# Kernel optimization log

Measured on AMD Instinct MI355X. Metric: run time of the kernel, lower is better.

The kernel has to match this reference:

```python
import jax, jax.numpy as jnp
import numpy as np

N, E, D_IN, D_H, N_CLASSES = 50000, 800000, 128, 128, 40
D_OUT = D_H // 2
LN_EPS = 1e-5


def _seg_mean(msgs, dst, n_nodes):
    # mean aggregation over incoming edges; isolated nodes get 0 (like PyG mean)
    s = jax.ops.segment_sum(msgs, dst, num_segments=n_nodes)
    cnt = jax.ops.segment_sum(jnp.ones((dst.shape[0], 1), msgs.dtype), dst, num_segments=n_nodes)
    return s / jnp.maximum(cnt, 1.0)


def _sage(x, src, dst, Wl, bl, Wr):
    # PyG SAGEConv(mean): lin_l(mean_j x_j) + lin_r(x_i); lin_l has bias, lin_r none
    agg = _seg_mean(x[src], dst, x.shape[0])  # [N, d_in]
    return agg @ Wl + bl + x @ Wr


def _layernorm(x, g, b):
    mu = jnp.mean(x, axis=-1, keepdims=True)
    var = jnp.mean(jnp.square(x - mu), axis=-1, keepdims=True)
    return (x - mu) * jax.lax.rsqrt(var + LN_EPS) * g + b


def setup_inputs() -> dict:
    key = jax.random.key(0)
    ks = jax.random.split(key, 20)
    sc = lambda d: 1.0 / np.sqrt(d)
    inp = {
        "x": jax.random.normal(ks[0], (N, D_IN), dtype=jnp.float32),
        "edge_index": jax.random.randint(ks[1], (2, E), 0, N, dtype=jnp.int32),
        # block1 (in==hidden -> proj is Identity)
        "Wl1": jax.random.normal(ks[2], (D_IN, D_H), jnp.float32) * sc(D_IN),
        "bl1": jnp.zeros((D_H,), jnp.float32),
        "Wr1": jax.random.normal(ks[3], (D_IN, D_H), jnp.float32) * sc(D_IN),
        "g1": jnp.ones((D_H,), jnp.float32),
        "b1": jnp.zeros((D_H,), jnp.float32),
        # block2
        "Wl2": jax.random.normal(ks[4], (D_H, D_H), jnp.float32) * sc(D_H),
        "bl2": jnp.zeros((D_H,), jnp.float32),
        "Wr2": jax.random.normal(ks[5], (D_H, D_H), jnp.float32) * sc(D_H),
        "g2": jnp.ones((D_H,), jnp.float32),
        "b2": jnp.zeros((D_H,), jnp.float32),
        # conv_out: hidden -> hidden//2
        "Wl3": jax.random.normal(ks[6], (D_H, D_OUT), jnp.float32) * sc(D_H),
        "bl3": jnp.zeros((D_OUT,), jnp.float32),
        "Wr3": jax.random.normal(ks[7], (D_H, D_OUT), jnp.float32) * sc(D_H),
        # classifier: LayerNorm(D_OUT) + Linear(D_OUT, n_classes)
        "gc": jnp.ones((D_OUT,), jnp.float32),
        "bc": jnp.zeros((D_OUT,), jnp.float32),
        "Wc": jax.random.normal(ks[8], (D_OUT, N_CLASSES), jnp.float32) * sc(D_OUT),
        "bcls": jnp.zeros((N_CLASSES,), jnp.float32),
    }
    return inp


def reference(x, edge_index, Wl1, bl1, Wr1, g1, b1, Wl2, bl2, Wr2, g2, b2,
              Wl3, bl3, Wr3, gc, bc, Wc, bcls):
    src, dst = edge_index[0], edge_index[1]
    # block1: SAGE -> LN -> GELU -> (dropout eval=identity) -> +x (proj=Identity)
    h = _sage(x, src, dst, Wl1, bl1, Wr1)
    x = jax.nn.gelu(_layernorm(h, g1, b1), approximate=False) + x
    # block2
    h = _sage(x, src, dst, Wl2, bl2, Wr2)
    x = jax.nn.gelu(_layernorm(h, g2, b2), approximate=False) + x
    # conv_out + GELU
    x = jax.nn.gelu(_sage(x, src, dst, Wl3, bl3, Wr3), approximate=False)
    # classifier: LN then Linear
    return _layernorm(x, gc, bc) @ Wc + bcls
```

## Files before the change

kernel.cpp:

```cpp
#include <hip/hip_runtime.h>
#include <math.h>


typedef __attribute__((ext_vector_type(8))) short bf16x8;
typedef __attribute__((ext_vector_type(4))) float f32x4;

#define NWG 256
#define NBK 196
#define CAP2 6144

__device__ inline float gelu_f(float x) {
    float u = x * (1.0f + 0.044715f * x * x);
    return x / (1.0f + __expf(-1.5957691216057308f * u));
}

__device__ inline ushort f2b(float f) {
    uint u = __float_as_uint(f);
    u += 0x7fffu + ((u >> 16) & 1u);
    return (ushort)(u >> 16);
}

__device__ inline float b2f(ushort h) { return __uint_as_float((uint)h << 16); }


__global__ __launch_bounds__(256) void k_hist(const int* __restrict__ dst, int e,
                                              int* __restrict__ cnts) {
    __shared__ int h[NBK];
    const int tid = threadIdx.x;
    const int wg = blockIdx.x;
    for (int i = tid; i < NBK; i += 256) h[i] = 0;
    __syncthreads();
    const int ch = (e + NWG - 1) / NWG;
    const int lo = wg * ch;
    const int hi = min(e, lo + ch);
    for (int i = lo + tid; i < hi; i += 256) atomicAdd(&h[dst[i] >> 8], 1);
    __syncthreads();
    for (int i = tid; i < NBK; i += 256) cnts[i * NWG + wg] = h[i];
}

__global__ __launch_bounds__(256) void k_scanP1(const int* __restrict__ in,
                                                int* __restrict__ out,
                                                int* __restrict__ part, int m) {
    __shared__ int sm[256];
    const int tid = threadIdx.x;
    const int base = blockIdx.x * 1024 + tid * 4;
    int4 v = make_int4(0, 0, 0, 0);
    if (base + 3 < m) {
        v = *(const int4*)(in + base);
    } else {
        if (base + 0 < m) v.x = in[base + 0];
        if (base + 1 < m) v.y = in[base + 1];
        if (base + 2 < m) v.z = in[base + 2];
        if (base + 3 < m) v.w = in[base + 3];
    }
    int s = v.x + v.y + v.z + v.w;
    sm[tid] = s;
    __syncthreads();
#pragma unroll
    for (int d = 1; d < 256; d <<= 1) {
        int add = (tid >= d) ? sm[tid - d] : 0;
        __syncthreads();
        sm[tid] += add;
        __syncthreads();
    }
    int ex = (tid ? sm[tid - 1] : 0);
    if (base + 0 < m) out[base + 0] = ex;
    ex += v.x;
    if (base + 1 < m) out[base + 1] = ex;
    ex += v.y;
    if (base + 2 < m) out[base + 2] = ex;
    ex += v.z;
    if (base + 3 < m) out[base + 3] = ex;
    if (tid == 255) part[blockIdx.x] = sm[255];
}

__global__ __launch_bounds__(256) void k_scanP2(int* __restrict__ out,
                                                const int* __restrict__ part, int m) {
    const int tid = threadIdx.x;
    const int bid = blockIdx.x;
    const int lane = tid & 63;
    int s = 0;
    for (int j = lane; j < bid; j += 64) s += part[j];
#pragma unroll
    for (int d = 32; d > 0; d >>= 1) s += __shfl_xor(s, d);
    const int i0 = bid * 1024 + tid * 4;
#pragma unroll
    for (int j = 0; j < 4; ++j) {
        int i = i0 + j;
        if (i < m) out[i] += s;
    }
}

__global__ __launch_bounds__(256) void k_scat(const int* __restrict__ src,
                                              const int* __restrict__ dst, int e,
                                              const int* __restrict__ bases,
                                              uint* __restrict__ pairs) {
    __shared__ int cur[NBK];
    const int tid = threadIdx.x;
    const int wg = blockIdx.x;
    for (int i = tid; i < NBK; i += 256) cur[i] = bases[i * NWG + wg];
    __syncthreads();
    const int ch = (e + NWG - 1) / NWG;
    const int lo = wg * ch;
    const int hi = min(e, lo + ch);
    for (int i = lo + tid; i < hi; i += 256) {
        int d = dst[i];
        int pos = atomicAdd(&cur[d >> 8], 1);
        pairs[pos] = (uint)src[i] | ((uint)(d & 255) << 16);
    }
}

__global__ __launch_bounds__(256) void k_sortC(const uint* __restrict__ pairs,
                                               const int* __restrict__ bases, int e,
                                               int* __restrict__ csr, int* __restrict__ off,
                                               int* __restrict__ cntout, int n) {
    __shared__ int hist[256];
    __shared__ int curl[256];
    __shared__ int sm[256];
    __shared__ int buf[CAP2];
    const int bk = blockIdx.x;
    const int tid = threadIdx.x;
    const int start = bases[bk * NWG];
    const int end = (bk == NBK - 1) ? e : bases[(bk + 1) * NWG];
    int m = end - start;
    if (m > CAP2) m = CAP2;

    hist[tid] = 0;
    __syncthreads();
    for (int i = tid; i < m; i += 256) atomicAdd(&hist[(pairs[start + i] >> 16) & 255], 1);
    __syncthreads();
    int v = hist[tid];
    sm[tid] = v;
    __syncthreads();
#pragma unroll
    for (int d = 1; d < 256; d <<= 1) {
        int add = (tid >= d) ? sm[tid - d] : 0;
        __syncthreads();
        sm[tid] += add;
        __syncthreads();
    }
    int excl = sm[tid] - v;
    int node = (bk << 8) + tid;
    if (node < n) {
        off[node] = start + excl;
        cntout[node] = v;
    }
    curl[tid] = excl;
    __syncthreads();
    for (int i = tid; i < m; i += 256) {
        uint w = pairs[start + i];
        int pos = atomicAdd(&curl[(w >> 16) & 255], 1);
        buf[pos] = (int)(w & 0xffffu);
    }
    __syncthreads();
    for (int i = tid; i < m; i += 256) csr[start + i] = buf[i];
}


__global__ void k_cast(const float* __restrict__ in, ushort* __restrict__ out, int nvec4) {
    int t = blockIdx.x * blockDim.x + threadIdx.x;
    int stride = gridDim.x * blockDim.x;
    for (int i = t; i < nvec4; i += stride) {
        float4 v = ((const float4*)in)[i];
        ushort4 o;
        o.x = f2b(v.x);
        o.y = f2b(v.y);
        o.z = f2b(v.z);
        o.w = f2b(v.w);
        ((ushort4*)out)[i] = o;
    }
}

__global__ void k_wprep(const float* __restrict__ Wl, const float* __restrict__ Wr,
                        int KH, int C, ushort* __restrict__ Wt) {
    int t = blockIdx.x * blockDim.x + threadIdx.x;
    int total = C * 2 * KH;
    if (t >= total) return;
    int c = t / (2 * KH), k = t % (2 * KH);
    float v = (k < KH) ? Wl[(size_t)k * C + c] : Wr[(size_t)(k - KH) * C + c];
    Wt[t] = f2b(v);
}

__global__ void k_wprepC(const float* __restrict__ Wc, ushort* __restrict__ Wct) {
    int t = blockIdx.x * blockDim.x + threadIdx.x;
    if (t >= 64 * 64) return;
    int c = t >> 6, k = t & 63;
    float v = (c < 40) ? Wc[k * 40 + c] : 0.f;
    Wct[t] = f2b(v);
}


__global__ __launch_bounds__(256) void k_agg(const ushort* __restrict__ X,
                                             const int* __restrict__ off,
                                             const int* __restrict__ cnt,
                                             const int* __restrict__ csr,
                                             ushort* __restrict__ agg, int n) {
    const int wave = threadIdx.x >> 6;
    const int lane = threadIdx.x & 63;
    const int base = blockIdx.x * 32 + wave * 8;
#pragma unroll 1
    for (int j = 0; j < 8; ++j) {
        const int i = base + j;
        if (i >= n) return;
        int s0 = off[i];
        int deg = cnt[i];
        int c = 0;
        if (lane < deg) c = csr[s0 + lane];
        float a0 = 0.f, a1 = 0.f;
        const int dcap = deg < 64 ? deg : 64;
        int t = 0;
        for (; t + 3 < dcap; t += 4) {
            int i0 = __shfl(c, t), i1 = __shfl(c, t + 1);
            int i2 = __shfl(c, t + 2), i3 = __shfl(c, t + 3);
            uint u0 = *((const uint*)(X + (size_t)i0 * 128) + lane);
            uint u1 = *((const uint*)(X + (size_t)i1 * 128) + lane);
            uint u2 = *((const uint*)(X + (size_t)i2 * 128) + lane);
            uint u3 = *((const uint*)(X + (size_t)i3 * 128) + lane);
            a0 += __uint_as_float(u0 << 16) + __uint_as_float(u1 << 16) +
                  __uint_as_float(u2 << 16) + __uint_as_float(u3 << 16);
            a1 += __uint_as_float(u0 & 0xffff0000u) + __uint_as_float(u1 & 0xffff0000u) +
                  __uint_as_float(u2 & 0xffff0000u) + __uint_as_float(u3 & 0xffff0000u);
        }
        for (; t < dcap; ++t) {
            uint u0 = *((const uint*)(X + (size_t)__shfl(c, t) * 128) + lane);
            a0 += __uint_as_float(u0 << 16);
            a1 += __uint_as_float(u0 & 0xffff0000u);
        }
        for (int tt = s0 + 64; tt < s0 + deg; ++tt) {
            uint u0 = *((const uint*)(X + (size_t)csr[tt] * 128) + lane);
            a0 += __uint_as_float(u0 << 16);
            a1 += __uint_as_float(u0 & 0xffff0000u);
        }
        float inv = 1.0f / (float)(deg > 1 ? deg : 1);
        uint pk = (uint)f2b(a0 * inv) | ((uint)f2b(a1 * inv) << 16);
        *((uint*)(agg + (size_t)i * 128) + lane) = pk;
    }
}


template <int DOUT, int EPI>
__global__ __launch_bounds__(256) void k_gemm(
    const ushort* __restrict__ Agg, const ushort* __restrict__ Xb,
    const ushort* __restrict__ Wt, const float* __restrict__ bias,
    const float* __restrict__ g, const float* __restrict__ b,
    ushort* __restrict__ OutB, int n) {
    constexpr int CT = DOUT / 64;
    const int tid = threadIdx.x;
    const int wave = tid >> 6;
    const int lane = tid & 63;
    const int l16 = lane & 15;
    const int g4 = lane >> 4;
    const int row0 = blockIdx.x * 32;

    __shared__ __align__(16) ushort As[32 * 256];

    int colv[CT];
#pragma unroll
    for (int ct = 0; ct < CT; ++ct) colv[ct] = (wave * CT + ct) * 16 + l16;

    bf16x8 bfr[CT][8];
#pragma unroll
    for (int ct = 0; ct < CT; ++ct) {
        const ushort* wp = Wt + (size_t)colv[ct] * 256 + g4 * 8;
#pragma unroll
        for (int ks = 0; ks < 8; ++ks) bfr[ct][ks] = *(const bf16x8*)(wp + ks * 32);
    }

    {
        const int row = tid >> 3;
        const int jj = tid & 7;
        int gr = row0 + row;
        if (gr > n - 1) gr = n - 1;
        const ushort* pa = Agg + (size_t)gr * 128;
        const ushort* pb = Xb + (size_t)gr * 128;
        uint4 v0 = *(const uint4*)(pa + jj * 8);
        uint4 v1 = *(const uint4*)(pa + (jj + 8) * 8);
        uint4 v2 = *(const uint4*)(pb + jj * 8);
        uint4 v3 = *(const uint4*)(pb + (jj + 8) * 8);
        const int sw = (row & 7) << 4;
        char* lb = (char*)As + row * 512;
        *(uint4*)(lb + ((jj * 16) ^ sw)) = v0;
        *(uint4*)(lb + (((jj + 8) * 16) ^ sw)) = v1;
        *(uint4*)(lb + (((jj + 16) * 16) ^ sw)) = v2;
        *(uint4*)(lb + (((jj + 24) * 16) ^ sw)) = v3;
    }

    float biasv[CT], gv[CT], bbv[CT];
#pragma unroll
    for (int ct = 0; ct < CT; ++ct) {
        biasv[ct] = bias[colv[ct]];
        gv[ct] = g[colv[ct]];
        bbv[ct] = b[colv[ct]];
    }

    __syncthreads();

    f32x4 acc[2][CT];
#pragma unroll
    for (int rt = 0; rt < 2; ++rt)
#pragma unroll
        for (int ct = 0; ct < CT; ++ct) {
            acc[rt][ct][0] = 0.f;
            acc[rt][ct][1] = 0.f;
            acc[rt][ct][2] = 0.f;
            acc[rt][ct][3] = 0.f;
        }
#pragma unroll
    for (int ks = 0; ks < 8; ++ks) {
        bf16x8 a[2];
#pragma unroll
        for (int rt = 0; rt < 2; ++rt) {
            const int row = rt * 16 + l16;
            a[rt] = *(const bf16x8*)((const char*)As + row * 512 +
                                     ((ks * 64 + g4 * 16) ^ ((row & 7) << 4)));
        }
#pragma unroll
        for (int rt = 0; rt < 2; ++rt)
#pragma unroll
            for (int ct = 0; ct < CT; ++ct)
                acc[rt][ct] = __builtin_amdgcn_mfma_f32_16x16x32_bf16(a[rt], bfr[ct][ks],
                                                                     acc[rt][ct], 0, 0, 0);
    }

    __shared__ float sP[32][4];
    __shared__ float qP[32][4];
    float v[2][4][CT];
    float sv[2][4], qv[2][4];
#pragma unroll
    for (int rt = 0; rt < 2; ++rt)
#pragma unroll
        for (int reg = 0; reg < 4; ++reg) {
            float s = 0.f, q = 0.f;
#pragma unroll
            for (int ct = 0; ct < CT; ++ct) {
                float t = acc[rt][ct][reg] + biasv[ct];
                if (EPI == 3) t = gelu_f(t);
                v[rt][reg][ct] = t;
                s += t;
                q += t * t;
            }
            sv[rt][reg] = s;
            qv[rt][reg] = q;
        }
#pragma unroll
    for (int m = 1; m < 16; m <<= 1)
#pragma unroll
        for (int rt = 0; rt < 2; ++rt)
#pragma unroll
            for (int reg = 0; reg < 4; ++reg) {
                sv[rt][reg] += __shfl_xor(sv[rt][reg], m);
                qv[rt][reg] += __shfl_xor(qv[rt][reg], m);
            }
    if (l16 == 0) {
#pragma unroll
        for (int rt = 0; rt < 2; ++rt)
#pragma unroll
            for (int reg = 0; reg < 4; ++reg) {
                int rib = rt * 16 + g4 * 4 + reg;
                sP[rib][wave] = sv[rt][reg];
                qP[rib][wave] = qv[rt][reg];
            }
    }
    __syncthreads();
#pragma unroll
    for (int rt = 0; rt < 2; ++rt) {
#pragma unroll
        for (int reg = 0; reg < 4; ++reg) {
            int rib = rt * 16 + g4 * 4 + reg;
            float s = sP[rib][0] + sP[rib][1] + sP[rib][2] + sP[rib][3];
            float q = qP[rib][0] + qP[rib][1] + qP[rib][2] + qP[rib][3];
            float mu = s * (1.0f / (float)DOUT);
            float var = q * (1.0f / (float)DOUT) - mu * mu;
            float rs = rsqrtf(fmaxf(var, 0.f) + 1e-5f);
            int r = row0 + rib;
            if (r >= n) continue;
#pragma unroll
            for (int ct = 0; ct < CT; ++ct) {
                float y = (v[rt][reg][ct] - mu) * rs * gv[ct] + bbv[ct];
                if (EPI == 1) {
                    ushort rh = *(const ushort*)((const char*)As + rib * 512 +
                                                 ((256 + 2 * colv[ct]) ^ ((rib & 7) << 4)));
                    y = gelu_f(y) + b2f(rh);
                }
                OutB[(size_t)r * DOUT + colv[ct]] = f2b(y);
            }
        }
    }
}


__global__ __launch_bounds__(256) void k_mm(const ushort* __restrict__ Y,
                                            const ushort* __restrict__ Wct,
                                            const float* __restrict__ bcls,
                                            float* __restrict__ Out, int n) {
    const int tid = threadIdx.x;
    const int wave = tid >> 6;
    const int lane = tid & 63;
    const int l16 = lane & 15;
    const int g4 = lane >> 4;
    const int row0 = blockIdx.x * 32;
    const int col = wave * 16 + l16;

    bf16x8 bfr[2];
#pragma unroll
    for (int ks = 0; ks < 2; ++ks)
        bfr[ks] = *(const bf16x8*)(Wct + (size_t)col * 64 + ks * 32 + g4 * 8);

    f32x4 acc[2];
#pragma unroll
    for (int rt = 0; rt < 2; ++rt) {
        acc[rt][0] = 0.f;
        acc[rt][1] = 0.f;
        acc[rt][2] = 0.f;
        acc[rt][3] = 0.f;
    }

    int arow[2];
#pragma unroll
    for (int rt = 0; rt < 2; ++rt) {
        int r = row0 + rt * 16 + l16;
        arow[rt] = (r < n) ? r : (n - 1);
    }

#pragma unroll
    for (int ks = 0; ks < 2; ++ks)
#pragma unroll
        for (int rt = 0; rt < 2; ++rt) {
            bf16x8 a = *(const bf16x8*)(Y + (size_t)arow[rt] * 64 + ks * 32 + g4 * 8);
            acc[rt] = __builtin_amdgcn_mfma_f32_16x16x32_bf16(a, bfr[ks], acc[rt], 0, 0, 0);
        }

    const float bcv = (col < 40) ? bcls[col] : 0.f;
#pragma unroll
    for (int rt = 0; rt < 2; ++rt)
#pragma unroll
        for (int reg = 0; reg < 4; ++reg) {
            int r = row0 + rt * 16 + g4 * 4 + reg;
            if (r < n && col < 40) Out[(size_t)r * 40 + col] = acc[rt][reg] + bcv;
        }
}


extern "C" void kernel_launch(void* const* d_in, const int* in_sizes, int n_in,
                              void* d_out, int out_size, void* d_ws, size_t ws_size,
                              hipStream_t stream) {
    const float* x   = (const float*)d_in[0];
    const int* ei    = (const int*)d_in[1];
    const float* Wl1 = (const float*)d_in[2];
    const float* bl1 = (const float*)d_in[3];
    const float* Wr1 = (const float*)d_in[4];
    const float* g1  = (const float*)d_in[5];
    const float* b1  = (const float*)d_in[6];
    const float* Wl2 = (const float*)d_in[7];
    const float* bl2 = (const float*)d_in[8];
    const float* Wr2 = (const float*)d_in[9];
    const float* g2  = (const float*)d_in[10];
    const float* b2  = (const float*)d_in[11];
    const float* Wl3 = (const float*)d_in[12];
    const float* bl3 = (const float*)d_in[13];
    const float* Wr3 = (const float*)d_in[14];
    const float* gc  = (const float*)d_in[15];
    const float* bc  = (const float*)d_in[16];
    const float* Wc  = (const float*)d_in[17];
    const float* bcls= (const float*)d_in[18];

    const int n = in_sizes[0] / 128;
    const int e = in_sizes[1] / 2;
    const int* src = ei;
    const int* dst = ei + e;

    char* w = (char*)d_ws;
    size_t o = 0;
    auto alloc = [&](size_t bytes) -> char* {
        char* p = w + o;
        o = (o + bytes + 511) & ~(size_t)511;
        return p;
    };
    int* cnts    = (int*)alloc((size_t)NBK * NWG * 4);
    int* bases   = (int*)alloc((size_t)NBK * NWG * 4);
    int* part    = (int*)alloc(256 * 4);
    uint* pairs  = (uint*)alloc((size_t)e * 4);
    int* csr     = (int*)alloc((size_t)e * 4);
    int* off     = (int*)alloc((size_t)n * 4);
    int* cnt     = (int*)alloc((size_t)n * 4);
    ushort* xB   = (ushort*)alloc((size_t)n * 128 * 2);
    ushort* aggB = (ushort*)alloc((size_t)n * 128 * 2);
    ushort* xaB  = (ushort*)alloc((size_t)n * 128 * 2);
    ushort* xbB  = (ushort*)alloc((size_t)n * 128 * 2);
    ushort* yB   = (ushort*)alloc((size_t)n * 64 * 2);
    ushort* W1t  = (ushort*)alloc((size_t)128 * 256 * 2);
    ushort* W2t  = (ushort*)alloc((size_t)128 * 256 * 2);
    ushort* W3t  = (ushort*)alloc((size_t)64 * 256 * 2);
    ushort* Wct  = (ushort*)alloc((size_t)64 * 64 * 2);
    (void)ws_size;

    const int m = NBK * NWG;
    const int sblk = (m + 1023) / 1024;
    k_hist<<<NWG, 256, 0, stream>>>(dst, e, cnts);
    k_scanP1<<<sblk, 256, 0, stream>>>(cnts, bases, part, m);
    k_scanP2<<<sblk, 256, 0, stream>>>(bases, part, m);
    k_scat<<<NWG, 256, 0, stream>>>(src, dst, e, bases, pairs);
    k_sortC<<<NBK, 256, 0, stream>>>(pairs, bases, e, csr, off, cnt, n);

    k_cast<<<2048, 256, 0, stream>>>(x, xB, n * 128 / 4);
    k_wprep<<<(128 * 256 + 255) / 256, 256, 0, stream>>>(Wl1, Wr1, 128, 128, W1t);
    k_wprep<<<(128 * 256 + 255) / 256, 256, 0, stream>>>(Wl2, Wr2, 128, 128, W2t);
    k_wprep<<<(64 * 256 + 255) / 256, 256, 0, stream>>>(Wl3, Wr3, 128, 64, W3t);
    k_wprepC<<<16, 256, 0, stream>>>(Wc, Wct);

    const int gg = (n + 31) / 32;

    k_agg<<<gg, 256, 0, stream>>>(xB, off, cnt, csr, aggB, n);
    k_gemm<128, 1><<<gg, 256, 0, stream>>>(aggB, xB, W1t, bl1, g1, b1, xaB, n);
    k_agg<<<gg, 256, 0, stream>>>(xaB, off, cnt, csr, aggB, n);
    k_gemm<128, 1><<<gg, 256, 0, stream>>>(aggB, xaB, W2t, bl2, g2, b2, xbB, n);
    k_agg<<<gg, 256, 0, stream>>>(xbB, off, cnt, csr, aggB, n);
    k_gemm<64, 3><<<gg, 256, 0, stream>>>(aggB, xbB, W3t, bl3, gc, bc, yB, n);
    k_mm<<<gg, 256, 0, stream>>>(yB, Wct, bcls, (float*)d_out, n);
}
```

Before: 207.5 us.

## Process two row tiles per GEMM block with prefetched double-buffered LDS

Each k_gemm block now handles 64 rows as two 32-row tiles instead of one. The weight fragments held in registers are loaded once and reused for both tiles. The second tile's global loads are issued into registers while the first tile is being computed, and each tile gets its own LDS buffer. This targets the per-block cost of reloading weights and overlaps global memory latency with MFMA and epilogue work, at the price of a halved grid, more LDS, and higher register pressure.

Result: slower. 223.7 us (+7.8%).

```diff
diff --git a/kernel.cpp b/kernel.cpp
--- a/kernel.cpp
+++ b/kernel.cpp
@@ -250,9 +250,10 @@
     const int lane = tid & 63;
     const int l16 = lane & 15;
     const int g4 = lane >> 4;
-    const int row0 = blockIdx.x * 32;
-
-    __shared__ __align__(16) ushort As[32 * 256];
+
+    __shared__ __align__(16) ushort As[2][32 * 256];
+    __shared__ float sP[32][4];
+    __shared__ float qP[32][4];
 
     int colv[CT];
 #pragma unroll
@@ -265,26 +266,6 @@
 #pragma unroll
         for (int ks = 0; ks < 8; ++ks) bfr[ct][ks] = *(const bf16x8*)(wp + ks * 32);
     }
-
-    {
-        const int row = tid >> 3;
-        const int jj = tid & 7;
-        int gr = row0 + row;
-        if (gr > n - 1) gr = n - 1;
-        const ushort* pa = Agg + (size_t)gr * 128;
-        const ushort* pb = Xb + (size_t)gr * 128;
-        uint4 v0 = *(const uint4*)(pa + jj * 8);
-        uint4 v1 = *(const uint4*)(pa + (jj + 8) * 8);
-        uint4 v2 = *(const uint4*)(pb + jj * 8);
-        uint4 v3 = *(const uint4*)(pb + (jj + 8) * 8);
-        const int sw = (row & 7) << 4;
-        char* lb = (char*)As + row * 512;
-        *(uint4*)(lb + ((jj * 16) ^ sw)) = v0;
-        *(uint4*)(lb + (((jj + 8) * 16) ^ sw)) = v1;
-        *(uint4*)(lb + (((jj + 16) * 16) ^ sw)) = v2;
-        *(uint4*)(lb + (((jj + 24) * 16) ^ sw)) = v3;
-    }
-
     float biasv[CT], gv[CT], bbv[CT];
 #pragma unroll
     for (int ct = 0; ct < CT; ++ct) {
@@ -293,96 +274,123 @@
         bbv[ct] = b[colv[ct]];
     }
 
-    __syncthreads();
-
-    f32x4 acc[2][CT];
-#pragma unroll
-    for (int rt = 0; rt < 2; ++rt)
-#pragma unroll
-        for (int ct = 0; ct < CT; ++ct) {
-            acc[rt][ct][0] = 0.f;
-            acc[rt][ct][1] = 0.f;
-            acc[rt][ct][2] = 0.f;
-            acc[rt][ct][3] = 0.f;
-        }
-#pragma unroll
-    for (int ks = 0; ks < 8; ++ks) {
-        bf16x8 a[2];
+    const int srow = tid >> 3;
+    const int sjj = tid & 7;
+    auto ldtile = [&](int row0, uint4* v) {
+        int gr = row0 + srow;
+        if (gr > n - 1) gr = n - 1;
+        const ushort* pa = Agg + (size_t)gr * 128;
+        const ushort* pb = Xb + (size_t)gr * 128;
+        v[0] = *(const uint4*)(pa + sjj * 8);
+        v[1] = *(const uint4*)(pa + (sjj + 8) * 8);
+        v[2] = *(const uint4*)(pb + sjj * 8);
+        v[3] = *(const uint4*)(pb + (sjj + 8) * 8);
+    };
+
+    uint4 ld[4];
+    ldtile(blockIdx.x * 64, ld);
+
+#pragma unroll
+    for (int t = 0; t < 2; ++t) {
+        const int row0 = blockIdx.x * 64 + t * 32;
+        {
+            const int sw = (srow & 7) << 4;
+            char* lb = (char*)As[t] + srow * 512;
+            *(uint4*)(lb + ((sjj * 16) ^ sw)) = ld[0];
+            *(uint4*)(lb + (((sjj + 8) * 16) ^ sw)) = ld[1];
+            *(uint4*)(lb + (((sjj + 16) * 16) ^ sw)) = ld[2];
+            *(uint4*)(lb + (((sjj + 24) * 16) ^ sw)) = ld[3];
+        }
+        if (t == 0) ldtile(blockIdx.x * 64 + 32, ld);
+        __syncthreads();
+
+        f32x4 acc[2][CT];
+#pragma unroll
+        for (int rt = 0; rt < 2; ++rt)
+#pragma unroll
+            for (int ct = 0; ct < CT; ++ct) {
+                acc[rt][ct][0] = 0.f;
+                acc[rt][ct][1] = 0.f;
+                acc[rt][ct][2] = 0.f;
+                acc[rt][ct][3] = 0.f;
+            }
+#pragma unroll
+        for (int ks = 0; ks < 8; ++ks) {
+            bf16x8 a[2];
+#pragma unroll
+            for (int rt = 0; rt < 2; ++rt) {
+                const int row = rt * 16 + l16;
+                a[rt] = *(const bf16x8*)((const char*)As[t] + row * 512 +
+                                         ((ks * 64 + g4 * 16) ^ ((row & 7) << 4)));
+            }
+#pragma unroll
+            for (int rt = 0; rt < 2; ++rt)
+#pragma unroll
+                for (int ct = 0; ct < CT; ++ct)
+                    acc[rt][ct] = __builtin_amdgcn_mfma_f32_16x16x32_bf16(a[rt], bfr[ct][ks],
+                                                                         acc[rt][ct], 0, 0, 0);
+        }
+
+        float v[2][4][CT];
+        float sv[2][4], qv[2][4];
+#pragma unroll
+        for (int rt = 0; rt < 2; ++rt)
+#pragma unroll
+            for (int reg = 0; reg < 4; ++reg) {
+                float s = 0.f, q = 0.f;
+#pragma unroll
+                for (int ct = 0; ct < CT; ++ct) {
+                    float tv = acc[rt][ct][reg] + biasv[ct];
+                    if (EPI == 3) tv = gelu_f(tv);
+                    v[rt][reg][ct] = tv;
+                    s += tv;
+                    q += tv * tv;
+                }
+                sv[rt][reg] = s;
+                qv[rt][reg] = q;
+            }
+#pragma unroll
+        for (int m = 1; m < 16; m <<= 1)
+#pragma unroll
+            for (int rt = 0; rt < 2; ++rt)
+#pragma unroll
+                for (int reg = 0; reg < 4; ++reg) {
+                    sv[rt][reg] += __shfl_xor(sv[rt][reg], m);
+                    qv[rt][reg] += __shfl_xor(qv[rt][reg], m);
+                }
+        if (l16 == 0) {
+#pragma unroll
+            for (int rt = 0; rt < 2; ++rt)
+#pragma unroll
+                for (int reg = 0; reg < 4; ++reg) {
+                    int rib = rt * 16 + g4 * 4 + reg;
+                    sP[rib][wave] = sv[rt][reg];
+                    qP[rib][wave] = qv[rt][reg];
+                }
+        }
+        __syncthreads();
 #pragma unroll
         for (int rt = 0; rt < 2; ++rt) {
-            const int row = rt * 16 + l16;
-            a[rt] = *(const bf16x8*)((const char*)As + row * 512 +
-                                     ((ks * 64 + g4 * 16) ^ ((row & 7) << 4)));
-        }
-#pragma unroll
-        for (int rt = 0; rt < 2; ++rt)
-#pragma unroll
-            for (int ct = 0; ct < CT; ++ct)
-                acc[rt][ct] = __builtin_amdgcn_mfma_f32_16x16x32_bf16(a[rt], bfr[ct][ks],
-                                                                     acc[rt][ct], 0, 0, 0);
-    }
-
-    __shared__ float sP[32][4];
-    __shared__ float qP[32][4];
-    float v[2][4][CT];
-    float sv[2][4], qv[2][4];
-#pragma unroll
-    for (int rt = 0; rt < 2; ++rt)
-#pragma unroll
-        for (int reg = 0; reg < 4; ++reg) {
-            float s = 0.f, q = 0.f;
-#pragma unroll
-            for (int ct = 0; ct < CT; ++ct) {
-                float t = acc[rt][ct][reg] + biasv[ct];
-                if (EPI == 3) t = gelu_f(t);
-                v[rt][reg][ct] = t;
-                s += t;
-                q += t * t;
-            }
-            sv[rt][reg] = s;
-            qv[rt][reg] = q;
-        }
-#pragma unroll
-    for (int m = 1; m < 16; m <<= 1)
-#pragma unroll
-        for (int rt = 0; rt < 2; ++rt)
-#pragma unroll
-            for (int reg = 0; reg < 4; ++reg) {
-                sv[rt][reg] += __shfl_xor(sv[rt][reg], m);
-                qv[rt][reg] += __shfl_xor(qv[rt][reg], m);
-            }
-    if (l16 == 0) {
-#pragma unroll
-        for (int rt = 0; rt < 2; ++rt)
 #pragma unroll
             for (int reg = 0; reg < 4; ++reg) {
                 int rib = rt * 16 + g4 * 4 + reg;
-                sP[rib][wave] = sv[rt][reg];
-                qP[rib][wave] = qv[rt][reg];
-            }
-    }
-    __syncthreads();
-#pragma unroll
-    for (int rt = 0; rt < 2; ++rt) {
-#pragma unroll
-        for (int reg = 0; reg < 4; ++reg) {
-            int rib = rt * 16 + g4 * 4 + reg;
-            float s = sP[rib][0] + sP[rib][1] + sP[rib][2] + sP[rib][3];
-            float q = qP[rib][0] + qP[rib][1] + qP[rib][2] + qP[rib][3];
-            float mu = s * (1.0f / (float)DOUT);
-            float var = q * (1.0f / (float)DOUT) - mu * mu;
-            float rs = rsqrtf(fmaxf(var, 0.f) + 1e-5f);
-            int r = row0 + rib;
-            if (r >= n) continue;
-#pragma unroll
-            for (int ct = 0; ct < CT; ++ct) {
-                float y = (v[rt][reg][ct] - mu) * rs * gv[ct] + bbv[ct];
-                if (EPI == 1) {
-                    ushort rh = *(const ushort*)((const char*)As + rib * 512 +
-                                                 ((256 + 2 * colv[ct]) ^ ((rib & 7) << 4)));
-                    y = gelu_f(y) + b2f(rh);
+                float s = sP[rib][0] + sP[rib][1] + sP[rib][2] + sP[rib][3];
+                float q = qP[rib][0] + qP[rib][1] + qP[rib][2] + qP[rib][3];
+                float mu = s * (1.0f / (float)DOUT);
+                float var = q * (1.0f / (float)DOUT) - mu * mu;
+                float rs = rsqrtf(fmaxf(var, 0.f) + 1e-5f);
+                int r = row0 + rib;
+                if (r >= n) continue;
+#pragma unroll
+                for (int ct = 0; ct < CT; ++ct) {
+                    float y = (v[rt][reg][ct] - mu) * rs * gv[ct] + bbv[ct];
+                    if (EPI == 1) {
+                        ushort rh = *(const ushort*)((const char*)As[t] + rib * 512 +
+                                                     ((256 + 2 * colv[ct]) ^ ((rib & 7) << 4)));
+                        y = gelu_f(y) + b2f(rh);
+                    }
+                    OutB[(size_t)r * DOUT + colv[ct]] = f2b(y);
                 }
-                OutB[(size_t)r * DOUT + colv[ct]] = f2b(y);
             }
         }
     }
@@ -508,13 +516,14 @@
     k_wprep<<<(64 * 256 + 255) / 256, 256, 0, stream>>>(Wl3, Wr3, 128, 64, W3t);
     k_wprepC<<<16, 256, 0, stream>>>(Wc, Wct);
 
-    const int gg = (n + 31) / 32;
-
-    k_agg<<<gg, 256, 0, stream>>>(xB, off, cnt, csr, aggB, n);
+    const int ga = (n + 31) / 32;
+    const int gg = (n + 63) / 64;
+
+    k_agg<<<ga, 256, 0, stream>>>(xB, off, cnt, csr, aggB, n);
     k_gemm<128, 1><<<gg, 256, 0, stream>>>(aggB, xB, W1t, bl1, g1, b1, xaB, n);
-    k_agg<<<gg, 256, 0, stream>>>(xaB, off, cnt, csr, aggB, n);
+    k_agg<<<ga, 256, 0, stream>>>(xaB, off, cnt, csr, aggB, n);
     k_gemm<128, 1><<<gg, 256, 0, stream>>>(aggB, xaB, W2t, bl2, g2, b2, xbB, n);
-    k_agg<<<gg, 256, 0, stream>>>(xbB, off, cnt, csr, aggB, n);
+    k_agg<<<ga, 256, 0, stream>>>(xbB, off, cnt, csr, aggB, n);
     k_gemm<64, 3><<<gg, 256, 0, stream>>>(aggB, xbB, W3t, bl3, gc, bc, yB, n);
-    k_mm<<<gg, 256, 0, stream>>>(yB, Wct, bcls, (float*)d_out, n);
-}
+    k_mm<<<ga, 256, 0, stream>>>(yB, Wct, bcls, (float*)d_out, n);
+}
```

## Fuse classifier matmul into final SAGE gemm and use direct global-to-LDS loads

Applied to the files above, without the earlier changes.

Fuses the final classifier Linear into the third gemm kernel's epilogue. The LayerNorm output is staged in a swizzled LDS tile and multiplied there, which removes the intermediate yB buffer and one kernel launch. Also replaces the register-staged A-tile load with global_load_lds direct-to-LDS transfers, swizzling on the source address. This adds LDS use and a barrier in the EPI==3 kernel, and relies on correct vmcnt waiting before the LDS reads.

New measurement: 202.0 us. 1.03x faster.

```diff
diff --git a/kernel.cpp b/kernel.cpp
--- a/kernel.cpp
+++ b/kernel.cpp
@@ -4,6 +4,9 @@
 
 typedef __attribute__((ext_vector_type(8))) short bf16x8;
 typedef __attribute__((ext_vector_type(4))) float f32x4;
+
+#define AS1 __attribute__((address_space(1)))
+#define AS3 __attribute__((address_space(3)))
 
 #define NWG 256
 #define NBK 196
@@ -243,7 +246,11 @@
     const ushort* __restrict__ Agg, const ushort* __restrict__ Xb,
     const ushort* __restrict__ Wt, const float* __restrict__ bias,
     const float* __restrict__ g, const float* __restrict__ b,
-    ushort* __restrict__ OutB, int n) {
+    ushort* __restrict__ OutB,
+    const ushort* __restrict__ Wct,
+    const float* __restrict__ bcls,
+    float* __restrict__ OutF,
+    int n) {
     constexpr int CT = DOUT / 64;
     const int tid = threadIdx.x;
     const int wave = tid >> 6;
@@ -253,6 +260,25 @@
     const int row0 = blockIdx.x * 32;
 
     __shared__ __align__(16) ushort As[32 * 256];
+    __shared__ float sP[32][4];
+    __shared__ float qP[32][4];
+    __shared__ __align__(16) ushort Ys[EPI == 3 ? 32 * 64 : 1];
+
+    {
+        const int slot = lane & 31;
+#pragma unroll
+        for (int i = 0; i < 4; ++i) {
+            const int rr = (wave * 4 + i) * 2 + (lane >> 5);
+            int gr = row0 + rr;
+            if (gr > n - 1) gr = n - 1;
+            const int srcb = (slot * 16) ^ ((rr & 7) << 4);
+            const char* gp = (srcb < 256)
+                                 ? (const char*)Agg + (size_t)gr * 256 + srcb
+                                 : (const char*)Xb + (size_t)gr * 256 + (srcb - 256);
+            char* lp = (char*)As + (wave * 4 + i) * 1024;
+            __builtin_amdgcn_global_load_lds((const AS1 void*)gp, (AS3 void*)lp, 16, 0, 0);
+        }
+    }
 
     int colv[CT];
 #pragma unroll
@@ -265,26 +291,6 @@
 #pragma unroll
         for (int ks = 0; ks < 8; ++ks) bfr[ct][ks] = *(const bf16x8*)(wp + ks * 32);
     }
-
-    {
-        const int row = tid >> 3;
-        const int jj = tid & 7;
-        int gr = row0 + row;
-        if (gr > n - 1) gr = n - 1;
-        const ushort* pa = Agg + (size_t)gr * 128;
-        const ushort* pb = Xb + (size_t)gr * 128;
-        uint4 v0 = *(const uint4*)(pa + jj * 8);
-        uint4 v1 = *(const uint4*)(pa + (jj + 8) * 8);
-        uint4 v2 = *(const uint4*)(pb + jj * 8);
-        uint4 v3 = *(const uint4*)(pb + (jj + 8) * 8);
-        const int sw = (row & 7) << 4;
-        char* lb = (char*)As + row * 512;
-        *(uint4*)(lb + ((jj * 16) ^ sw)) = v0;
-        *(uint4*)(lb + (((jj + 8) * 16) ^ sw)) = v1;
-        *(uint4*)(lb + (((jj + 16) * 16) ^ sw)) = v2;
-        *(uint4*)(lb + (((jj + 24) * 16) ^ sw)) = v3;
-    }
-
     float biasv[CT], gv[CT], bbv[CT];
 #pragma unroll
     for (int ct = 0; ct < CT; ++ct) {
@@ -322,8 +328,6 @@
                                                                      acc[rt][ct], 0, 0, 0);
     }
 
-    __shared__ float sP[32][4];
-    __shared__ float qP[32][4];
     float v[2][4][CT];
     float sv[2][4], qv[2][4];
 #pragma unroll
@@ -333,11 +337,11 @@
             float s = 0.f, q = 0.f;
 #pragma unroll
             for (int ct = 0; ct < CT; ++ct) {
-                float t = acc[rt][ct][reg] + biasv[ct];
-                if (EPI == 3) t = gelu_f(t);
-                v[rt][reg][ct] = t;
-                s += t;
-                q += t * t;
+                float tv = acc[rt][ct][reg] + biasv[ct];
+                if (EPI == 3) tv = gelu_f(tv);
+                v[rt][reg][ct] = tv;
+                s += tv;
+                q += tv * tv;
             }
             sv[rt][reg] = s;
             qv[rt][reg] = q;
@@ -362,6 +366,7 @@
             }
     }
     __syncthreads();
+
 #pragma unroll
     for (int rt = 0; rt < 2; ++rt) {
 #pragma unroll
@@ -373,71 +378,57 @@
             float var = q * (1.0f / (float)DOUT) - mu * mu;
             float rs = rsqrtf(fmaxf(var, 0.f) + 1e-5f);
             int r = row0 + rib;
-            if (r >= n) continue;
 #pragma unroll
             for (int ct = 0; ct < CT; ++ct) {
                 float y = (v[rt][reg][ct] - mu) * rs * gv[ct] + bbv[ct];
                 if (EPI == 1) {
-                    ushort rh = *(const ushort*)((const char*)As + rib * 512 +
-                                                 ((256 + 2 * colv[ct]) ^ ((rib & 7) << 4)));
-                    y = gelu_f(y) + b2f(rh);
+                    if (r < n) {
+                        ushort rh = *(const ushort*)((const char*)As + rib * 512 +
+                                                     ((256 + 2 * colv[ct]) ^ ((rib & 7) << 4)));
+                        y = gelu_f(y) + b2f(rh);
+                        OutB[(size_t)r * DOUT + colv[ct]] = f2b(y);
+                    }
+                } else {
+                    *(ushort*)((char*)Ys + rib * 128 +
+                               ((2 * colv[ct]) ^ ((rib & 7) << 4))) = f2b(y);
                 }
-                OutB[(size_t)r * DOUT + colv[ct]] = f2b(y);
             }
         }
     }
-}
-
-
-__global__ __launch_bounds__(256) void k_mm(const ushort* __restrict__ Y,
-                                            const ushort* __restrict__ Wct,
-                                            const float* __restrict__ bcls,
-                                            float* __restrict__ Out, int n) {
-    const int tid = threadIdx.x;
-    const int wave = tid >> 6;
-    const int lane = tid & 63;
-    const int l16 = lane & 15;
-    const int g4 = lane >> 4;
-    const int row0 = blockIdx.x * 32;
-    const int col = wave * 16 + l16;
-
-    bf16x8 bfr[2];
-#pragma unroll
-    for (int ks = 0; ks < 2; ++ks)
-        bfr[ks] = *(const bf16x8*)(Wct + (size_t)col * 64 + ks * 32 + g4 * 8);
-
-    f32x4 acc[2];
-#pragma unroll
-    for (int rt = 0; rt < 2; ++rt) {
-        acc[rt][0] = 0.f;
-        acc[rt][1] = 0.f;
-        acc[rt][2] = 0.f;
-        acc[rt][3] = 0.f;
-    }
-
-    int arow[2];
-#pragma unroll
-    for (int rt = 0; rt < 2; ++rt) {
-        int r = row0 + rt * 16 + l16;
-        arow[rt] = (r < n) ? r : (n - 1);
-    }
-
-#pragma unroll
-    for (int ks = 0; ks < 2; ++ks)
+
+    if (EPI == 3) {
+        __syncthreads();
+        const int col = wave * 16 + l16;
+        bf16x8 b2r[2];
+#pragma unroll
+        for (int ks = 0; ks < 2; ++ks)
+            b2r[ks] = *(const bf16x8*)(Wct + (size_t)col * 64 + ks * 32 + g4 * 8);
+        f32x4 acc2[2];
 #pragma unroll
         for (int rt = 0; rt < 2; ++rt) {
-            bf16x8 a = *(const bf16x8*)(Y + (size_t)arow[rt] * 64 + ks * 32 + g4 * 8);
-            acc[rt] = __builtin_amdgcn_mfma_f32_16x16x32_bf16(a, bfr[ks], acc[rt], 0, 0, 0);
-        }
-
-    const float bcv = (col < 40) ? bcls[col] : 0.f;
-#pragma unroll
-    for (int rt = 0; rt < 2; ++rt)
-#pragma unroll
-        for (int reg = 0; reg < 4; ++reg) {
-            int r = row0 + rt * 16 + g4 * 4 + reg;
-            if (r < n && col < 40) Out[(size_t)r * 40 + col] = acc[rt][reg] + bcv;
-        }
+            acc2[rt][0] = 0.f;
+            acc2[rt][1] = 0.f;
+            acc2[rt][2] = 0.f;
+            acc2[rt][3] = 0.f;
+        }
+#pragma unroll
+        for (int ks = 0; ks < 2; ++ks)
+#pragma unroll
+            for (int rt = 0; rt < 2; ++rt) {
+                const int row = rt * 16 + l16;
+                bf16x8 a = *(const bf16x8*)((const char*)Ys + row * 128 +
+                                            ((ks * 64 + g4 * 16) ^ ((row & 7) << 4)));
+                acc2[rt] = __builtin_amdgcn_mfma_f32_16x16x32_bf16(a, b2r[ks], acc2[rt], 0, 0, 0);
+            }
+        const float bcv = (col < 40) ? bcls[col] : 0.f;
+#pragma unroll
+        for (int rt = 0; rt < 2; ++rt)
+#pragma unroll
+            for (int reg = 0; reg < 4; ++reg) {
+                int r = row0 + rt * 16 + g4 * 4 + reg;
+                if (r < n && col < 40) OutF[(size_t)r * 40 + col] = acc2[rt][reg] + bcv;
+            }
+    }
 }
 
 
@@ -487,7 +478,6 @@
     ushort* aggB = (ushort*)alloc((size_t)n * 128 * 2);
     ushort* xaB  = (ushort*)alloc((size_t)n * 128 * 2);
     ushort* xbB  = (ushort*)alloc((size_t)n * 128 * 2);
-    ushort* yB   = (ushort*)alloc((size_t)n * 64 * 2);
     ushort* W1t  = (ushort*)alloc((size_t)128 * 256 * 2);
     ushort* W2t  = (ushort*)alloc((size_t)128 * 256 * 2);
     ushort* W3t  = (ushort*)alloc((size_t)64 * 256 * 2);
@@ -511,10 +501,12 @@
     const int gg = (n + 31) / 32;
 
     k_agg<<<gg, 256, 0, stream>>>(xB, off, cnt, csr, aggB, n);
-    k_gemm<128, 1><<<gg, 256, 0, stream>>>(aggB, xB, W1t, bl1, g1, b1, xaB, n);
+    k_gemm<128, 1><<<gg, 256, 0, stream>>>(aggB, xB, W1t, bl1, g1, b1, xaB,
+                                           nullptr, nullptr, nullptr, n);
     k_agg<<<gg, 256, 0, stream>>>(xaB, off, cnt, csr, aggB, n);
-    k_gemm<128, 1><<<gg, 256, 0, stream>>>(aggB, xaB, W2t, bl2, g2, b2, xbB, n);
+    k_gemm<128, 1><<<gg, 256, 0, stream>>>(aggB, xaB, W2t, bl2, g2, b2, xbB,
+                                           nullptr, nullptr, nullptr, n);
     k_agg<<<gg, 256, 0, stream>>>(xbB, off, cnt, csr, aggB, n);
-    k_gemm<64, 3><<<gg, 256, 0, stream>>>(aggB, xbB, W3t, bl3, gc, bc, yB, n);
-    k_mm<<<gg, 256, 0, stream>>>(yB, Wct, bcls, (float*)d_out, n);
-}
+    k_gemm<64, 3><<<gg, 256, 0, stream>>>(aggB, xbB, W3t, bl3, gc, bc, nullptr,
+                                          Wct, bcls, (float*)d_out, n);
+}
```

## Reorder SAGE layers to transform first, then aggregate with fused LayerNorm epilogue

Applied to the files above, without the earlier changes.

Uses the linearity of mean aggregation to compute X@[Wl|Wr] first, in a plain MFMA GEMM that writes a wide bf16 intermediate. Neighbour aggregation then runs on the projected features, and bias, LayerNorm, GELU and the residual are fused into that gather kernel using wave-level reductions. In the third layer the gather reads 64-wide rows instead of 128-wide ones, which cuts the dominant irregular memory traffic. The cost is writing a wider intermediate, strided gathers over 512-byte rows, and rounding to bf16 before aggregation, which slightly changes numerics.

Result: slower. 220.2 us (+6.1%).

```diff
diff --git a/kernel.cpp b/kernel.cpp
--- a/kernel.cpp
+++ b/kernel.cpp
@@ -4,6 +4,9 @@
 
 typedef __attribute__((ext_vector_type(8))) short bf16x8;
 typedef __attribute__((ext_vector_type(4))) float f32x4;
+
+#define AS1 __attribute__((address_space(1)))
+#define AS3 __attribute__((address_space(3)))
 
 #define NWG 256
 #define NBK 196
@@ -12,6 +15,12 @@
 __device__ inline float gelu_f(float x) {
     float u = x * (1.0f + 0.044715f * x * x);
     return x / (1.0f + __expf(-1.5957691216057308f * u));
+}
+
+__device__ inline float wave_sum(float v) {
+#pragma unroll
+    for (int d = 32; d > 0; d >>= 1) v += __shfl_xor(v, d);
+    return v;
 }
 
 __device__ inline ushort f2b(float f) {
@@ -171,13 +180,13 @@
     }
 }
 
-__global__ void k_wprep(const float* __restrict__ Wl, const float* __restrict__ Wr,
-                        int KH, int C, ushort* __restrict__ Wt) {
+__global__ void k_wprepW(const float* __restrict__ Wl, const float* __restrict__ Wr,
+                         int CH, int K, ushort* __restrict__ Wt) {
     int t = blockIdx.x * blockDim.x + threadIdx.x;
-    int total = C * 2 * KH;
+    int total = 2 * CH * K;
     if (t >= total) return;
-    int c = t / (2 * KH), k = t % (2 * KH);
-    float v = (k < KH) ? Wl[(size_t)k * C + c] : Wr[(size_t)(k - KH) * C + c];
+    int c = t / K, k = t % K;
+    float v = (c < CH) ? Wl[(size_t)k * CH + c] : Wr[(size_t)k * CH + (c - CH)];
     Wt[t] = f2b(v);
 }
 
@@ -190,14 +199,103 @@
 }
 
 
-__global__ __launch_bounds__(256) void k_agg(const ushort* __restrict__ X,
-                                             const int* __restrict__ off,
-                                             const int* __restrict__ cnt,
-                                             const int* __restrict__ csr,
-                                             ushort* __restrict__ agg, int n) {
+template <int CW>
+__global__ __launch_bounds__(256) void k_gemmW(const ushort* __restrict__ X,
+                                               const ushort* __restrict__ Wt,
+                                               ushort* __restrict__ Y, int n) {
+    constexpr int CT = CW / 64;
+    const int tid = threadIdx.x;
+    const int wave = tid >> 6;
+    const int lane = tid & 63;
+    const int l16 = lane & 15;
+    const int g4 = lane >> 4;
+    const int row0 = blockIdx.x * 32;
+
+    __shared__ __align__(16) ushort As[32 * 128];
+
+    {
+        const int slot = lane & 15;
+#pragma unroll
+        for (int i = 0; i < 2; ++i) {
+            const int rr = (wave * 2 + i) * 4 + (lane >> 4);
+            int gr = row0 + rr;
+            if (gr > n - 1) gr = n - 1;
+            const int srcb = (slot * 16) ^ ((rr & 7) << 4);
+            const char* gp = (const char*)X + (size_t)gr * 256 + srcb;
+            char* lp = (char*)As + (wave * 2 + i) * 1024;
+            __builtin_amdgcn_global_load_lds((const AS1 void*)gp, (AS3 void*)lp, 16, 0, 0);
+        }
+    }
+
+    int colv[CT];
+#pragma unroll
+    for (int ct = 0; ct < CT; ++ct) colv[ct] = (wave * CT + ct) * 16 + l16;
+
+    bf16x8 bfr[CT][4];
+#pragma unroll
+    for (int ct = 0; ct < CT; ++ct) {
+        const ushort* wp = Wt + (size_t)colv[ct] * 128 + g4 * 8;
+#pragma unroll
+        for (int ks = 0; ks < 4; ++ks) bfr[ct][ks] = *(const bf16x8*)(wp + ks * 32);
+    }
+
+    __syncthreads();
+
+    f32x4 acc[2][CT];
+#pragma unroll
+    for (int rt = 0; rt < 2; ++rt)
+#pragma unroll
+        for (int ct = 0; ct < CT; ++ct) {
+            acc[rt][ct][0] = 0.f;
+            acc[rt][ct][1] = 0.f;
+            acc[rt][ct][2] = 0.f;
+            acc[rt][ct][3] = 0.f;
+        }
+#pragma unroll
+    for (int ks = 0; ks < 4; ++ks) {
+        bf16x8 a[2];
+#pragma unroll
+        for (int rt = 0; rt < 2; ++rt) {
+            const int row = rt * 16 + l16;
+            a[rt] = *(const bf16x8*)((const char*)As + row * 256 +
+                                     ((ks * 64 + g4 * 16) ^ ((row & 7) << 4)));
+        }
+#pragma unroll
+        for (int rt = 0; rt < 2; ++rt)
+#pragma unroll
+            for (int ct = 0; ct < CT; ++ct)
+                acc[rt][ct] = __builtin_amdgcn_mfma_f32_16x16x32_bf16(a[rt], bfr[ct][ks],
+                                                                     acc[rt][ct], 0, 0, 0);
+    }
+
+#pragma unroll
+    for (int rt = 0; rt < 2; ++rt)
+#pragma unroll
+        for (int reg = 0; reg < 4; ++reg) {
+            int r = row0 + rt * 16 + g4 * 4 + reg;
+            if (r >= n) continue;
+#pragma unroll
+            for (int ct = 0; ct < CT; ++ct)
+                Y[(size_t)r * CW + colv[ct]] = f2b(acc[rt][ct][reg]);
+        }
+}
+
+
+__global__ __launch_bounds__(256) void k_aggpost(
+    const ushort* __restrict__ Y,
+    const ushort* __restrict__ Xres,
+    const int* __restrict__ off, const int* __restrict__ cnt,
+    const int* __restrict__ csr, const float* __restrict__ bl,
+    const float* __restrict__ g, const float* __restrict__ b,
+    ushort* __restrict__ Xout, int n) {
     const int wave = threadIdx.x >> 6;
     const int lane = threadIdx.x & 63;
     const int base = blockIdx.x * 32 + wave * 8;
+
+    const float2 blv = ((const float2*)bl)[lane];
+    const float2 gv = ((const float2*)g)[lane];
+    const float2 bv = ((const float2*)b)[lane];
+
 #pragma unroll 1
     for (int j = 0; j < 8; ++j) {
         const int i = base + j;
@@ -212,179 +310,84 @@
         for (; t + 3 < dcap; t += 4) {
             int i0 = __shfl(c, t), i1 = __shfl(c, t + 1);
             int i2 = __shfl(c, t + 2), i3 = __shfl(c, t + 3);
-            uint u0 = *((const uint*)(X + (size_t)i0 * 128) + lane);
-            uint u1 = *((const uint*)(X + (size_t)i1 * 128) + lane);
-            uint u2 = *((const uint*)(X + (size_t)i2 * 128) + lane);
-            uint u3 = *((const uint*)(X + (size_t)i3 * 128) + lane);
+            uint u0 = *((const uint*)(Y + (size_t)i0 * 256) + lane);
+            uint u1 = *((const uint*)(Y + (size_t)i1 * 256) + lane);
+            uint u2 = *((const uint*)(Y + (size_t)i2 * 256) + lane);
+            uint u3 = *((const uint*)(Y + (size_t)i3 * 256) + lane);
             a0 += __uint_as_float(u0 << 16) + __uint_as_float(u1 << 16) +
                   __uint_as_float(u2 << 16) + __uint_as_float(u3 << 16);
             a1 += __uint_as_float(u0 & 0xffff0000u) + __uint_as_float(u1 & 0xffff0000u) +
                   __uint_as_float(u2 & 0xffff0000u) + __uint_as_float(u3 & 0xffff0000u);
         }
         for (; t < dcap; ++t) {
-            uint u0 = *((const uint*)(X + (size_t)__shfl(c, t) * 128) + lane);
+            uint u0 = *((const uint*)(Y + (size_t)__shfl(c, t) * 256) + lane);
             a0 += __uint_as_float(u0 << 16);
             a1 += __uint_as_float(u0 & 0xffff0000u);
         }
         for (int tt = s0 + 64; tt < s0 + deg; ++tt) {
-            uint u0 = *((const uint*)(X + (size_t)csr[tt] * 128) + lane);
+            uint u0 = *((const uint*)(Y + (size_t)csr[tt] * 256) + lane);
             a0 += __uint_as_float(u0 << 16);
             a1 += __uint_as_float(u0 & 0xffff0000u);
         }
         float inv = 1.0f / (float)(deg > 1 ? deg : 1);
-        uint pk = (uint)f2b(a0 * inv) | ((uint)f2b(a1 * inv) << 16);
-        *((uint*)(agg + (size_t)i * 128) + lane) = pk;
-    }
-}
-
-
-template <int DOUT, int EPI>
-__global__ __launch_bounds__(256) void k_gemm(
-    const ushort* __restrict__ Agg, const ushort* __restrict__ Xb,
-    const ushort* __restrict__ Wt, const float* __restrict__ bias,
-    const float* __restrict__ g, const float* __restrict__ b,
-    ushort* __restrict__ OutB, int n) {
-    constexpr int CT = DOUT / 64;
-    const int tid = threadIdx.x;
-    const int wave = tid >> 6;
-    const int lane = tid & 63;
-    const int l16 = lane & 15;
-    const int g4 = lane >> 4;
-    const int row0 = blockIdx.x * 32;
-
-    __shared__ __align__(16) ushort As[32 * 256];
-
-    int colv[CT];
-#pragma unroll
-    for (int ct = 0; ct < CT; ++ct) colv[ct] = (wave * CT + ct) * 16 + l16;
-
-    bf16x8 bfr[CT][8];
-#pragma unroll
-    for (int ct = 0; ct < CT; ++ct) {
-        const ushort* wp = Wt + (size_t)colv[ct] * 256 + g4 * 8;
-#pragma unroll
-        for (int ks = 0; ks < 8; ++ks) bfr[ct][ks] = *(const bf16x8*)(wp + ks * 32);
-    }
-
-    {
-        const int row = tid >> 3;
-        const int jj = tid & 7;
-        int gr = row0 + row;
-        if (gr > n - 1) gr = n - 1;
-        const ushort* pa = Agg + (size_t)gr * 128;
-        const ushort* pb = Xb + (size_t)gr * 128;
-        uint4 v0 = *(const uint4*)(pa + jj * 8);
-        uint4 v1 = *(const uint4*)(pa + (jj + 8) * 8);
-        uint4 v2 = *(const uint4*)(pb + jj * 8);
-        uint4 v3 = *(const uint4*)(pb + (jj + 8) * 8);
-        const int sw = (row & 7) << 4;
-        char* lb = (char*)As + row * 512;
-        *(uint4*)(lb + ((jj * 16) ^ sw)) = v0;
-        *(uint4*)(lb + (((jj + 8) * 16) ^ sw)) = v1;
-        *(uint4*)(lb + (((jj + 16) * 16) ^ sw)) = v2;
-        *(uint4*)(lb + (((jj + 24) * 16) ^ sw)) = v3;
-    }
-
-    float biasv[CT], gv[CT], bbv[CT];
-#pragma unroll
-    for (int ct = 0; ct < CT; ++ct) {
-        biasv[ct] = bias[colv[ct]];
-        gv[ct] = g[colv[ct]];
-        bbv[ct] = b[colv[ct]];
-    }
-
-    __syncthreads();
-
-    f32x4 acc[2][CT];
-#pragma unroll
-    for (int rt = 0; rt < 2; ++rt)
-#pragma unroll
-        for (int ct = 0; ct < CT; ++ct) {
-            acc[rt][ct][0] = 0.f;
-            acc[rt][ct][1] = 0.f;
-            acc[rt][ct][2] = 0.f;
-            acc[rt][ct][3] = 0.f;
-        }
-#pragma unroll
-    for (int ks = 0; ks < 8; ++ks) {
-        bf16x8 a[2];
-#pragma unroll
-        for (int rt = 0; rt < 2; ++rt) {
-            const int row = rt * 16 + l16;
-            a[rt] = *(const bf16x8*)((const char*)As + row * 512 +
-                                     ((ks * 64 + g4 * 16) ^ ((row & 7) << 4)));
-        }
-#pragma unroll
-        for (int rt = 0; rt < 2; ++rt)
-#pragma unroll
-            for (int ct = 0; ct < CT; ++ct)
-                acc[rt][ct] = __builtin_amdgcn_mfma_f32_16x16x32_bf16(a[rt], bfr[ct][ks],
-                                                                     acc[rt][ct], 0, 0, 0);
-    }
-
-    __shared__ float sP[32][4];
-    __shared__ float qP[32][4];
-    float v[2][4][CT];
-    float sv[2][4], qv[2][4];
-#pragma unroll
-    for (int rt = 0; rt < 2; ++rt)
-#pragma unroll
-        for (int reg = 0; reg < 4; ++reg) {
-            float s = 0.f, q = 0.f;
-#pragma unroll
-            for (int ct = 0; ct < CT; ++ct) {
-                float t = acc[rt][ct][reg] + biasv[ct];
-                if (EPI == 3) t = gelu_f(t);
-                v[rt][reg][ct] = t;
-                s += t;
-                q += t * t;
-            }
-            sv[rt][reg] = s;
-            qv[rt][reg] = q;
-        }
-#pragma unroll
-    for (int m = 1; m < 16; m <<= 1)
-#pragma unroll
-        for (int rt = 0; rt < 2; ++rt)
-#pragma unroll
-            for (int reg = 0; reg < 4; ++reg) {
-                sv[rt][reg] += __shfl_xor(sv[rt][reg], m);
-                qv[rt][reg] += __shfl_xor(qv[rt][reg], m);
-            }
-    if (l16 == 0) {
-#pragma unroll
-        for (int rt = 0; rt < 2; ++rt)
-#pragma unroll
-            for (int reg = 0; reg < 4; ++reg) {
-                int rib = rt * 16 + g4 * 4 + reg;
-                sP[rib][wave] = sv[rt][reg];
-                qP[rib][wave] = qv[rt][reg];
-            }
-    }
-    __syncthreads();
-#pragma unroll
-    for (int rt = 0; rt < 2; ++rt) {
-#pragma unroll
-        for (int reg = 0; reg < 4; ++reg) {
-            int rib = rt * 16 + g4 * 4 + reg;
-            float s = sP[rib][0] + sP[rib][1] + sP[rib][2] + sP[rib][3];
-            float q = qP[rib][0] + qP[rib][1] + qP[rib][2] + qP[rib][3];
-            float mu = s * (1.0f / (float)DOUT);
-            float var = q * (1.0f / (float)DOUT) - mu * mu;
-            float rs = rsqrtf(fmaxf(var, 0.f) + 1e-5f);
-            int r = row0 + rib;
-            if (r >= n) continue;
-#pragma unroll
-            for (int ct = 0; ct < CT; ++ct) {
-                float y = (v[rt][reg][ct] - mu) * rs * gv[ct] + bbv[ct];
-                if (EPI == 1) {
-                    ushort rh = *(const ushort*)((const char*)As + rib * 512 +
-                                                 ((256 + 2 * colv[ct]) ^ ((rib & 7) << 4)));
-                    y = gelu_f(y) + b2f(rh);
-                }
-                OutB[(size_t)r * DOUT + colv[ct]] = f2b(y);
-            }
-        }
+        uint wv = *((const uint*)(Y + (size_t)i * 256 + 128) + lane);
+        float h0 = a0 * inv + __uint_as_float(wv << 16) + blv.x;
+        float h1 = a1 * inv + __uint_as_float(wv & 0xffff0000u) + blv.y;
+        float mu = wave_sum(h0 + h1) * (1.0f / 128.0f);
+        float d0 = h0 - mu, d1 = h1 - mu;
+        float var = wave_sum(d0 * d0 + d1 * d1) * (1.0f / 128.0f);
+        float rs = rsqrtf(var + 1e-5f);
+        uint rv = *((const uint*)(Xres + (size_t)i * 128) + lane);
+        float y0 = gelu_f(d0 * rs * gv.x + bv.x) + __uint_as_float(rv << 16);
+        float y1 = gelu_f(d1 * rs * gv.y + bv.y) + __uint_as_float(rv & 0xffff0000u);
+        uint pk = (uint)f2b(y0) | ((uint)f2b(y1) << 16);
+        *((uint*)(Xout + (size_t)i * 128) + lane) = pk;
+    }
+}
+
+
+__global__ __launch_bounds__(256) void k_aggpost3(
+    const ushort* __restrict__ Y,
+    const int* __restrict__ off, const int* __restrict__ cnt,
+    const int* __restrict__ csr, const float* __restrict__ bl3,
+    const float* __restrict__ gc, const float* __restrict__ bc,
+    ushort* __restrict__ Yout, int n) {
+    const int wave = threadIdx.x >> 6;
+    const int lane = threadIdx.x & 63;
+    const int base = blockIdx.x * 32 + wave * 8;
+
+    const float blv = bl3[lane];
+    const float gv = gc[lane];
+    const float bv = bc[lane];
+
+#pragma unroll 1
+    for (int j = 0; j < 8; ++j) {
+        const int i = base + j;
+        if (i >= n) return;
+        int s0 = off[i];
+        int deg = cnt[i];
+        int c = 0;
+        if (lane < deg) c = csr[s0 + lane];
+        float a = 0.f;
+        const int dcap = deg < 64 ? deg : 64;
+        int t = 0;
+        for (; t + 3 < dcap; t += 4) {
+            int i0 = __shfl(c, t), i1 = __shfl(c, t + 1);
+            int i2 = __shfl(c, t + 2), i3 = __shfl(c, t + 3);
+            a += b2f(Y[(size_t)i0 * 128 + lane]) + b2f(Y[(size_t)i1 * 128 + lane]) +
+                 b2f(Y[(size_t)i2 * 128 + lane]) + b2f(Y[(size_t)i3 * 128 + lane]);
+        }
+        for (; t < dcap; ++t) a += b2f(Y[(size_t)__shfl(c, t) * 128 + lane]);
+        for (int tt = s0 + 64; tt < s0 + deg; ++tt)
+            a += b2f(Y[(size_t)csr[tt] * 128 + lane]);
+        float inv = 1.0f / (float)(deg > 1 ? deg : 1);
+        float h = a * inv + b2f(Y[(size_t)i * 128 + 64 + lane]) + blv;
+        float hg = gelu_f(h);
+        float mu = wave_sum(hg) * (1.0f / 64.0f);
+        float d = hg - mu;
+        float var = wave_sum(d * d) * (1.0f / 64.0f);
+        float y = d * rsqrtf(var + 1e-5f) * gv + bv;
+        Yout[(size_t)i * 64 + lane] = f2b(y);
     }
 }
 
@@ -484,13 +487,13 @@
     int* off     = (int*)alloc((size_t)n * 4);
     int* cnt     = (int*)alloc((size_t)n * 4);
     ushort* xB   = (ushort*)alloc((size_t)n * 128 * 2);
-    ushort* aggB = (ushort*)alloc((size_t)n * 128 * 2);
+    ushort* Yb   = (ushort*)alloc((size_t)n * 256 * 2);
     ushort* xaB  = (ushort*)alloc((size_t)n * 128 * 2);
     ushort* xbB  = (ushort*)alloc((size_t)n * 128 * 2);
     ushort* yB   = (ushort*)alloc((size_t)n * 64 * 2);
-    ushort* W1t  = (ushort*)alloc((size_t)128 * 256 * 2);
-    ushort* W2t  = (ushort*)alloc((size_t)128 * 256 * 2);
-    ushort* W3t  = (ushort*)alloc((size_t)64 * 256 * 2);
+    ushort* W1c  = (ushort*)alloc((size_t)256 * 128 * 2);
+    ushort* W2c  = (ushort*)alloc((size_t)256 * 128 * 2);
+    ushort* W3c  = (ushort*)alloc((size_t)128 * 128 * 2);
     ushort* Wct  = (ushort*)alloc((size_t)64 * 64 * 2);
     (void)ws_size;
 
@@ -503,18 +506,18 @@
     k_sortC<<<NBK, 256, 0, stream>>>(pairs, bases, e, csr, off, cnt, n);
 
     k_cast<<<2048, 256, 0, stream>>>(x, xB, n * 128 / 4);
-    k_wprep<<<(128 * 256 + 255) / 256, 256, 0, stream>>>(Wl1, Wr1, 128, 128, W1t);
-    k_wprep<<<(128 * 256 + 255) / 256, 256, 0, stream>>>(Wl2, Wr2, 128, 128, W2t);
-    k_wprep<<<(64 * 256 + 255) / 256, 256, 0, stream>>>(Wl3, Wr3, 128, 64, W3t);
+    k_wprepW<<<(256 * 128 + 255) / 256, 256, 0, stream>>>(Wl1, Wr1, 128, 128, W1c);
+    k_wprepW<<<(256 * 128 + 255) / 256, 256, 0, stream>>>(Wl2, Wr2, 128, 128, W2c);
+    k_wprepW<<<(128 * 128 + 255) / 256, 256, 0, stream>>>(Wl3, Wr3, 64, 128, W3c);
     k_wprepC<<<16, 256, 0, stream>>>(Wc, Wct);
 
     const int gg = (n + 31) / 32;
 
-    k_agg<<<gg, 256, 0, stream>>>(xB, off, cnt, csr, aggB, n);
-    k_gemm<128, 1><<<gg, 256, 0, stream>>>(aggB, xB, W1t, bl1, g1, b1, xaB, n);
-    k_agg<<<gg, 256, 0, stream>>>(xaB, off, cnt, csr, aggB, n);
-    k_gemm<128, 1><<<gg, 256, 0, stream>>>(aggB, xaB, W2t, bl2, g2, b2, xbB, n);
-    k_agg<<<gg, 256, 0, stream>>>(xbB, off, cnt, csr, aggB, n);
-    k_gemm<64, 3><<<gg, 256, 0, stream>>>(aggB, xbB, W3t, bl3, gc, bc, yB, n);
+    k_gemmW<256><<<gg, 256, 0, stream>>>(xB, W1c, Yb, n);
+    k_aggpost<<<gg, 256, 0, stream>>>(Yb, xB, off, cnt, csr, bl1, g1, b1, xaB, n);
+    k_gemmW<256><<<gg, 256, 0, stream>>>(xaB, W2c, Yb, n);
+    k_aggpost<<<gg, 256, 0, stream>>>(Yb, xaB, off, cnt, csr, bl2, g2, b2, xbB, n);
+    k_gemmW<128><<<gg, 256, 0, stream>>>(xbB, W3c, Yb, n);
+    k_aggpost3<<<gg, 256, 0, stream>>>(Yb, off, cnt, csr, bl3, gc, bc, yB, n);
     k_mm<<<gg, 256, 0, stream>>>(yB, Wct, bcls, (float*)d_out, n);
 }
```
